# Kernel optimization log

Hardware: AMD Instinct MI355X
Metric: run time of the kernel (lower is better)

## Reference

```python
import jax, jax.numpy as jnp
import numpy as np

N_HEAD, D_MODEL, D_K, D_V = 16, 1024, 64, 64
B, S = 2, 2048
LN_EPS = 1e-5


def setup_inputs() -> dict:
    key = jax.random.key(0)
    ks = jax.random.split(key, 9)
    std_qk = np.sqrt(2.0 / (D_MODEL + D_K)).astype(np.float32)
    std_v = np.sqrt(2.0 / (D_MODEL + D_V)).astype(np.float32)
    return {
        "q": jax.random.normal(ks[0], (B, S, D_MODEL), jnp.float32),
        "k": jax.random.normal(ks[1], (B, S, D_MODEL), jnp.float32),
        "v": jax.random.normal(ks[2], (B, S, D_MODEL), jnp.float32),
        # nn.Linear weights stored as [out, in]; we apply x @ W.T
        "w_qs": jax.random.normal(ks[3], (N_HEAD * D_K, D_MODEL), jnp.float32) * std_qk,
        "w_ks": jax.random.normal(ks[4], (N_HEAD * D_K, D_MODEL), jnp.float32) * std_qk,
        "w_vs": jax.random.normal(ks[5], (N_HEAD * D_V, D_MODEL), jnp.float32) * std_v,
        "fc_w": jax.random.normal(ks[6], (D_MODEL, N_HEAD * D_V), jnp.float32) * np.sqrt(2.0 / (D_MODEL + N_HEAD * D_V)).astype(np.float32),
        "fc_b": jnp.zeros((D_MODEL,), jnp.float32),
        "ln_g": jnp.ones((D_MODEL,), jnp.float32),
        "ln_b": jnp.zeros((D_MODEL,), jnp.float32),
    }


def reference(q, k, v, w_qs, w_ks, w_vs, fc_w, fc_b, ln_g, ln_b):
    temperature = jnp.asarray(np.power(D_K, 0.5), q.dtype)
    residual = q
    # projections -> [b, s, h, d]
    qh = (q @ w_qs.T).reshape(B, S, N_HEAD, D_K)
    kh = (k @ w_ks.T).reshape(B, S, N_HEAD, D_K)
    vh = (v @ w_vs.T).reshape(B, S, N_HEAD, D_V)
    # scaled dot-product attention (dropout = identity in eval)
    attn = jnp.einsum('bqhd,bkhd->bhqk', qh, kh) / temperature
    attn = jax.nn.softmax(attn, axis=-1)  # (log_softmax in source is unused)
    out = jnp.einsum('bhqk,bkhd->bqhd', attn, vh).reshape(B, S, N_HEAD * D_V)
    out = out @ fc_w.T + fc_b
    # layer norm over last dim
    x = out + residual
    mu = jnp.mean(x, axis=-1, keepdims=True)
    var = jnp.var(x, axis=-1, keepdims=True)
    return (x - mu) * jax.lax.rsqrt(var + LN_EPS) * ln_g + ln_b
```

## Files before the change

### kernel.cpp

```cpp
#include <hip/hip_runtime.h>
#include <hip/hip_bf16.h>

typedef _Float16 f16x8 __attribute__((ext_vector_type(8)));
typedef _Float16 f16x4 __attribute__((ext_vector_type(4)));
typedef _Float16 f16x2 __attribute__((ext_vector_type(2)));
typedef float f32x4 __attribute__((ext_vector_type(4)));
typedef float f32x16 __attribute__((ext_vector_type(16)));
typedef unsigned u32x4v __attribute__((ext_vector_type(4)));
typedef int i32x2 __attribute__((ext_vector_type(2)));

#define DEVI __device__ __forceinline__

constexpr int S_LEN = 2048;
constexpr int DM    = 1024;
constexpr int NH    = 16;
constexpr int DHD   = 64;
constexpr int MTOT  = 2 * S_LEN;

DEVI f32x4 mfma16(f16x8 a, f16x8 b, f32x4 c) {
    return __builtin_amdgcn_mfma_f32_16x16x32_f16(a, b, c, 0, 0, 0);
}
DEVI f32x16 mfma32(f16x8 a, f16x8 b, f32x16 c) {
    return __builtin_amdgcn_mfma_f32_32x32x16_f16(a, b, c, 0, 0, 0);
}

DEVI f16x2 cvt_pk(float a, float b) {
    return __builtin_bit_cast(f16x2, __builtin_amdgcn_cvt_pkrtz(a, b));
}

DEVI float fexp2(float x) {
#if __has_builtin(__builtin_amdgcn_exp2f)
    return __builtin_amdgcn_exp2f(x);
#else
    return exp2f(x);
#endif
}

DEVI void pl32swap(unsigned &a, unsigned &b) {
#if __has_builtin(__builtin_amdgcn_permlane32_swap)
    i32x2 r = __builtin_bit_cast(i32x2,
        __builtin_amdgcn_permlane32_swap((int)a, (int)b, false, false));
    a = (unsigned)r[0]; b = (unsigned)r[1];
#else
    int idx = (((int)(threadIdx.x & 63)) ^ 32) << 2;
    unsigned ra = (unsigned)__builtin_amdgcn_ds_bpermute(idx, (int)a);
    unsigned rb = (unsigned)__builtin_amdgcn_ds_bpermute(idx, (int)b);
    bool hi = (threadIdx.x & 32) != 0;
    unsigned na = hi ? rb : a;
    unsigned nb = hi ? b  : ra;
    a = na; b = nb;
#endif
}

DEVI void gload_lds16(const _Float16* g, _Float16* l) {
    __builtin_amdgcn_global_load_lds(
        (const __attribute__((address_space(1))) void*)g,
        (__attribute__((address_space(3))) void*)l, 16, 0, 0);
}

__global__ void k_conv(const float* __restrict__ s0, const float* __restrict__ s1,
                       const float* __restrict__ s2, const float* __restrict__ s3,
                       const float* __restrict__ s4, const float* __restrict__ s5,
                       const float* __restrict__ s6,
                       _Float16* __restrict__ d0, _Float16* __restrict__ d1,
                       _Float16* __restrict__ d2, _Float16* __restrict__ d3,
                       _Float16* __restrict__ d4, _Float16* __restrict__ d5,
                       _Float16* __restrict__ d6)
{
    const int QN4 = (MTOT * DM) / 4;
    const int WN4 = (DM * DM) / 4;
    const int TOT = 3 * QN4 + 4 * WN4;
    int stride = gridDim.x * blockDim.x;
    for (int i = blockIdx.x * blockDim.x + threadIdx.x; i < TOT; i += stride) {
        const float* s; _Float16* d; int off;
        if (i < 3 * QN4) {
            int t = i / QN4; off = i - t * QN4;
            s = t == 0 ? s0 : (t == 1 ? s1 : s2);
            d = t == 0 ? d0 : (t == 1 ? d1 : d2);
        } else {
            int j = i - 3 * QN4;
            int t = j / WN4; off = j - t * WN4;
            s = t == 0 ? s3 : (t == 1 ? s4 : (t == 2 ? s5 : s6));
            d = t == 0 ? d3 : (t == 1 ? d4 : (t == 2 ? d5 : d6));
        }
        float4 v = reinterpret_cast<const float4*>(s)[off];
        f16x4 o;
        o[0] = (_Float16)v.x; o[1] = (_Float16)v.y;
        o[2] = (_Float16)v.z; o[3] = (_Float16)v.w;
        *reinterpret_cast<f16x4*>(d + (size_t)off * 4) = o;
    }
}

DEVI void gemm_main(const _Float16* __restrict__ A, const _Float16* __restrict__ Bw,
                    int kLen, int ld, int m0, int n0, f32x4 (&acc)[4][4])
{
    __shared__ __align__(16) _Float16 As[128 * 64];
    __shared__ __align__(16) _Float16 Bs[128 * 64];

    const int tid = threadIdx.x;
    const int lane = tid & 63;
    const int w = tid >> 6;
    const int wm = w >> 1, wn = w & 1;
    const int lrow = lane & 15, lg = lane >> 4;
    const int srow = w * 8 + (lane >> 3);
    const int scol = ((lane & 7) ^ (srow & 7)) * 8;

#pragma unroll
    for (int i = 0; i < 4; i++)
#pragma unroll
        for (int j = 0; j < 4; j++) acc[i][j] = f32x4{0.f, 0.f, 0.f, 0.f};

    const _Float16* gA = A  + (size_t)(m0 + srow) * ld + scol;
    const _Float16* gB = Bw + (size_t)(n0 + srow) * ld + scol;

#pragma unroll
    for (int q = 0; q < 4; q++) {
        gload_lds16(gA + (size_t)q * 32 * ld, &As[(w * 8 + q * 32) * 64]);
        gload_lds16(gB + (size_t)q * 32 * ld, &Bs[(w * 8 + q * 32) * 64]);
    }

    const int kTiles = kLen >> 6;
    for (int kt = 0; kt < kTiles; ++kt) {
        __syncthreads();
#pragma unroll
        for (int kk = 0; kk < 2; kk++) {
            f16x8 af[4], bfm[4];
#pragma unroll
            for (int i = 0; i < 4; i++) {
                int row = wm * 64 + i * 16 + lrow;
                int slot = (kk * 4 + lg) ^ (row & 7);
                af[i] = *reinterpret_cast<const f16x8*>(As + row * 64 + slot * 8);
            }
#pragma unroll
            for (int j = 0; j < 4; j++) {
                int row = wn * 64 + j * 16 + lrow;
                int slot = (kk * 4 + lg) ^ (row & 7);
                bfm[j] = *reinterpret_cast<const f16x8*>(Bs + row * 64 + slot * 8);
            }
#pragma unroll
            for (int i = 0; i < 4; i++)
#pragma unroll
                for (int j = 0; j < 4; j++)
                    acc[i][j] = mfma16(af[i], bfm[j], acc[i][j]);
        }
        if (kt + 1 < kTiles) {
            asm volatile("s_waitcnt lgkmcnt(0)" ::: "memory");
            __builtin_amdgcn_s_barrier();
            const int ko = (kt + 1) * 64;
#pragma unroll
            for (int q = 0; q < 4; q++) {
                gload_lds16(gA + ko + (size_t)q * 32 * ld, &As[(w * 8 + q * 32) * 64]);
                gload_lds16(gB + ko + (size_t)q * 32 * ld, &Bs[(w * 8 + q * 32) * 64]);
            }
        }
    }
}

__global__ __launch_bounds__(256, 4)
void k_proj(const _Float16* __restrict__ qb, const _Float16* __restrict__ kb,
            const _Float16* __restrict__ vb,
            const _Float16* __restrict__ wq, const _Float16* __restrict__ wk,
            const _Float16* __restrict__ wv,
            _Float16* __restrict__ Qh, _Float16* __restrict__ Ks, _Float16* __restrict__ Vs)
{
    const int z = blockIdx.z;
    const _Float16* A = z == 0 ? qb : (z == 1 ? kb : vb);
    const _Float16* B = z == 0 ? wq : (z == 1 ? wk : wv);
    const int m0 = blockIdx.x * 128, n0 = blockIdx.y * 128;
    f32x4 acc[4][4];
    gemm_main(A, B, DM, DM, m0, n0, acc);

    const int lane = threadIdx.x & 63, w = threadIdx.x >> 6;
    const int wm = w >> 1, wn = w & 1;
    const int lrow = lane & 15, lg = lane >> 4;

    if (z == 0) {
        const float scale = 0.18033688011112042f;
#pragma unroll
        for (int i = 0; i < 4; i++)
#pragma unroll
            for (int j = 0; j < 4; j++) {
                int n = n0 + wn * 64 + j * 16 + lrow;
                int h = n >> 6, d = n & 63;
#pragma unroll
                for (int r = 0; r < 4; r++) {
                    int m = m0 + wm * 64 + i * 16 + lg * 4 + r;
                    int b = m >> 11, s = m & (S_LEN - 1);
                    size_t idx = ((size_t)(b * NH + h) * S_LEN + s) * DHD + d;
                    Qh[idx] = (_Float16)(acc[i][j][r] * scale);
                }
            }
    } else if (z == 1) {
#pragma unroll
        for (int i = 0; i < 4; i++)
#pragma unroll
            for (int j = 0; j < 4; j++) {
                int n = n0 + wn * 64 + j * 16 + lrow;
                int h = n >> 6, d = n & 63;
#pragma unroll
                for (int r = 0; r < 4; r++) {
                    int m = m0 + wm * 64 + i * 16 + lg * 4 + r;
                    int b = m >> 11, s = m & (S_LEN - 1);
                    size_t idx = (size_t)(b * NH + h) * 131072
                               + (size_t)(s >> 6) * 4096
                               + (d >> 3) * 512 + (s & 63) * 8 + (d & 7);
                    Ks[idx] = (_Float16)acc[i][j][r];
                }
            }
    } else {
#pragma unroll
        for (int i = 0; i < 4; i++) {
            int m = m0 + wm * 64 + i * 16 + lg * 4;
            int b = m >> 11, s = m & (S_LEN - 1);
#pragma unroll
            for (int j = 0; j < 4; j++) {
                int n = n0 + wn * 64 + j * 16 + lrow;
                int h = n >> 6, d = n & 63;
                size_t idx = (size_t)(b * NH + h) * 131072
                           + (size_t)(s >> 6) * 4096
                           + ((s >> 3) & 7) * 512 + d * 8 + (s & 7);
                f16x4 pk;
#pragma unroll
                for (int r = 0; r < 4; r++) pk[r] = (_Float16)acc[i][j][r];
                *reinterpret_cast<f16x4*>(Vs + idx) = pk;
            }
        }
    }
}

__global__ __launch_bounds__(256, 2)
void k_attn(const _Float16* __restrict__ Q, const _Float16* __restrict__ Ks,
            const _Float16* __restrict__ Vs, _Float16* __restrict__ Ob)
{
    __shared__ __align__(16) _Float16 Kl[2][4096];
    __shared__ __align__(16) _Float16 Vl[2][4096];

    const int tid  = threadIdx.x;
    const int lane = tid & 63, w = tid >> 6;
    const int l31  = lane & 31, hh = lane >> 5;

    const int raw  = blockIdx.x;
    const int swz  = (raw & 7) * 64 + (raw >> 3);
    const int bh   = swz >> 4;
    const int qblk = swz & 15;
    const int q0   = qblk * 128 + w * 32;

    const _Float16* Qb = Q  + (size_t)bh * S_LEN * DHD;
    const _Float16* gK = Ks + (size_t)bh * 131072 + w * 1024 + lane * 8;
    const _Float16* gV = Vs + (size_t)bh * 131072 + w * 1024 + lane * 8;

    f16x8 qf[4];
#pragma unroll
    for (int step = 0; step < 4; step++)
        qf[step] = *reinterpret_cast<const f16x8*>(
            Qb + (size_t)(q0 + l31) * DHD + step * 16 + hh * 8);

    f32x16 oacc[2], lacc, cinit;
#pragma unroll
    for (int i = 0; i < 16; i++) {
        oacc[0][i] = 0.f; oacc[1][i] = 0.f; lacc[i] = 0.f; cinit[i] = -7.f;
    }
    f16x8 vones;
#pragma unroll
    for (int i = 0; i < 8; i++) vones[i] = (_Float16)1.0f;

#pragma unroll
    for (int i = 0; i < 2; i++) {
        gload_lds16(gK + i * 512, &Kl[0][w * 1024 + i * 512]);
        gload_lds16(gV + i * 512, &Vl[0][w * 1024 + i * 512]);
    }

    for (int t = 0; t < 32; ++t) {
        const int cur = t & 1;
        asm volatile("s_waitcnt vmcnt(0) lgkmcnt(0)" ::: "memory");
        __builtin_amdgcn_s_barrier();
        if (t + 1 < 32) {
#pragma unroll
            for (int i = 0; i < 2; i++) {
                gload_lds16(gK + (t + 1) * 4096 + i * 512, &Kl[cur ^ 1][w * 1024 + i * 512]);
                gload_lds16(gV + (t + 1) * 4096 + i * 512, &Vl[cur ^ 1][w * 1024 + i * 512]);
            }
        }
        const _Float16* Kc = Kl[cur];
        const _Float16* Vc = Vl[cur];

        f32x16 sc0 = cinit, sc1 = cinit;
        __builtin_amdgcn_s_setprio(1);
#pragma unroll
        for (int step = 0; step < 4; step++) {
            const int sl = step * 2 + hh;
            f16x8 ka = *reinterpret_cast<const f16x8*>(Kc + sl * 512 + l31 * 8);
            f16x8 kb = *reinterpret_cast<const f16x8*>(Kc + sl * 512 + 256 + l31 * 8);
            sc0 = mfma32(ka, qf[step], sc0);
            sc1 = mfma32(kb, qf[step], sc1);
        }
        __builtin_amdgcn_s_setprio(0);

#pragma unroll
        for (int kb2 = 0; kb2 < 2; kb2++) {
            const f32x16 sc = kb2 ? sc1 : sc0;
            float e[16];
#pragma unroll
            for (int r = 0; r < 16; r++) e[r] = fexp2(sc[r]);
            unsigned Wa[4], Wb[4];
#pragma unroll
            for (int g = 0; g < 4; g++) {
                Wa[g] = __builtin_bit_cast(unsigned, cvt_pk(e[4 * g],     e[4 * g + 1]));
                Wb[g] = __builtin_bit_cast(unsigned, cvt_pk(e[4 * g + 2], e[4 * g + 3]));
            }
            pl32swap(Wa[0], Wa[1]); pl32swap(Wb[0], Wb[1]);
            pl32swap(Wa[2], Wa[3]); pl32swap(Wb[2], Wb[3]);
#pragma unroll
            for (int win = 0; win < 2; win++) {
                u32x4v fw = {Wa[2 * win], Wb[2 * win], Wa[2 * win + 1], Wb[2 * win + 1]};
                f16x8 pa = __builtin_bit_cast(f16x8, fw);
                const int slotb = kb2 * 4 + win * 2 + hh;
                __builtin_amdgcn_s_setprio(1);
#pragma unroll
                for (int dblk = 0; dblk < 2; dblk++) {
                    f16x8 vf = *reinterpret_cast<const f16x8*>(
                        Vc + slotb * 512 + dblk * 256 + l31 * 8);
                    oacc[dblk] = mfma32(pa, vf, oacc[dblk]);
                }
                lacc = mfma32(pa, vones, lacc);
                __builtin_amdgcn_s_setprio(0);
            }
        }
    }

    const int b = bh >> 4, h = bh & 15;
#pragma unroll
    for (int r = 0; r < 16; r++) {
        const float iq = 1.0f / lacc[r];
        const int qrow = q0 + (r & 3) + 8 * (r >> 2) + 4 * hh;
        const size_t m = (size_t)(b * S_LEN + qrow) * DM + h * 64;
        Ob[m + l31]      = (_Float16)(oacc[0][r] * iq);
        Ob[m + 32 + l31] = (_Float16)(oacc[1][r] * iq);
    }
}

__global__ __launch_bounds__(256, 4)
void k_fc(const _Float16* __restrict__ Ob, const _Float16* __restrict__ Wfc,
          const float* __restrict__ bias,
          _Float16* __restrict__ fcoA, _Float16* __restrict__ fcoB)
{
    const int z = blockIdx.z;
    const int m0 = blockIdx.x * 128, n0 = blockIdx.y * 128;
    f32x4 acc[4][4];
    gemm_main(Ob + z * 512, Wfc + z * 512, 512, DM, m0, n0, acc);

    _Float16* out = z == 0 ? fcoA : fcoB;
    const int lane = threadIdx.x & 63, w = threadIdx.x >> 6;
    const int wm = w >> 1, wn = w & 1;
    const int lrow = lane & 15, lg = lane >> 4;
#pragma unroll
    for (int j = 0; j < 4; j++) {
        int n = n0 + wn * 64 + j * 16 + lrow;
        float bv = (z == 0) ? bias[n] : 0.f;
#pragma unroll
        for (int i = 0; i < 4; i++)
#pragma unroll
            for (int r = 0; r < 4; r++) {
                int m = m0 + wm * 64 + i * 16 + lg * 4 + r;
                out[(size_t)m * DM + n] = (_Float16)(acc[i][j][r] + bv);
            }
    }
}

__global__ void k_ln(const _Float16* __restrict__ fa, const _Float16* __restrict__ fb,
                     const float* __restrict__ res,
                     const float* __restrict__ g, const float* __restrict__ be,
                     float* __restrict__ out)
{
    int row = blockIdx.x * 4 + (threadIdx.x >> 6);
    int lane = threadIdx.x & 63;
    const f16x4* ar = reinterpret_cast<const f16x4*>(fa + (size_t)row * DM);
    const f16x4* br2 = reinterpret_cast<const f16x4*>(fb + (size_t)row * DM);
    const float4* rr = reinterpret_cast<const float4*>(res + (size_t)row * DM);
    float4 v[4];
    float sum = 0.f, sq = 0.f;
#pragma unroll
    for (int t = 0; t < 4; t++) {
        f16x4 a = ar[lane + 64 * t];
        f16x4 bq = br2[lane + 64 * t];
        float4 b = rr[lane + 64 * t];
        float4 c = make_float4((float)a[0] + (float)bq[0] + b.x,
                               (float)a[1] + (float)bq[1] + b.y,
                               (float)a[2] + (float)bq[2] + b.z,
                               (float)a[3] + (float)bq[3] + b.w);
        v[t] = c;
        sum += c.x + c.y + c.z + c.w;
        sq  += c.x * c.x + c.y * c.y + c.z * c.z + c.w * c.w;
    }
#pragma unroll
    for (int o = 1; o < 64; o <<= 1) { sum += __shfl_xor(sum, o); sq += __shfl_xor(sq, o); }
    float mu = sum * (1.f / DM);
    float rstd = rsqrtf(fmaxf(sq * (1.f / DM) - mu * mu, 0.f) + 1e-5f);
    float4* orow = reinterpret_cast<float4*>(out + (size_t)row * DM);
    const float4* gr = reinterpret_cast<const float4*>(g);
    const float4* brr = reinterpret_cast<const float4*>(be);
#pragma unroll
    for (int t = 0; t < 4; t++) {
        float4 gg = gr[lane + 64 * t], bb = brr[lane + 64 * t];
        float4 c = v[t];
        orow[lane + 64 * t] = make_float4((c.x - mu) * rstd * gg.x + bb.x,
                                          (c.y - mu) * rstd * gg.y + bb.y,
                                          (c.z - mu) * rstd * gg.z + bb.z,
                                          (c.w - mu) * rstd * gg.w + bb.w);
    }
}

extern "C" void kernel_launch(void* const* d_in, const int* in_sizes, int n_in,
                              void* d_out, int out_size, void* d_ws, size_t ws_size,
                              hipStream_t stream)
{
    const float* q    = (const float*)d_in[0];
    const float* k    = (const float*)d_in[1];
    const float* v    = (const float*)d_in[2];
    const float* w_qs = (const float*)d_in[3];
    const float* w_ks = (const float*)d_in[4];
    const float* w_vs = (const float*)d_in[5];
    const float* fc_w = (const float*)d_in[6];
    const float* fc_b = (const float*)d_in[7];
    const float* ln_g = (const float*)d_in[8];
    const float* ln_b = (const float*)d_in[9];
    float* out = (float*)d_out;

    if (ws_size < (size_t)67108864) return;

    _Float16* ws  = (_Float16*)d_ws;
    _Float16* qbf = ws;
    _Float16* kbf = qbf + 4194304;
    _Float16* vbf = kbf + 4194304;
    _Float16* wq  = vbf + 4194304;
    _Float16* wk  = wq + 1048576;
    _Float16* wv  = wk + 1048576;
    _Float16* wfc = wv + 1048576;
    _Float16* Qh  = wfc + 1048576;
    _Float16* Ks  = Qh + 4194304;
    _Float16* Vs  = Ks + 4194304;
    _Float16* Ob  = Vs + 4194304;
    _Float16* fcoA = qbf;
    _Float16* fcoB = kbf;

    k_conv<<<2048, 256, 0, stream>>>(q, k, v, w_qs, w_ks, w_vs, fc_w,
                                     qbf, kbf, vbf, wq, wk, wv, wfc);
    k_proj<<<dim3(32, 8, 3), 256, 0, stream>>>(qbf, kbf, vbf, wq, wk, wv, Qh, Ks, Vs);
    k_attn<<<512, 256, 0, stream>>>(Qh, Ks, Vs, Ob);
    k_fc<<<dim3(32, 8, 2), 256, 0, stream>>>(Ob, wfc, fc_b, fcoA, fcoB);
    k_ln<<<1024, 256, 0, stream>>>(fcoA, fcoB, q, ln_g, ln_b, out);
}
```

Baseline: 125.2 us.

## Split attention over two key halves and combine partial sums in a new kernel

The attention kernel now splits the key/value sequence in two along a second grid dimension, doubling the block count, and raises the occupancy hint to four blocks per CU. Each half writes an unnormalized fp16 output plus its row sums, and a new combine kernel adds the halves and divides by the total sum. This works without rescaling because softmax uses a fixed shift (-7) rather than a running max. The aim is more parallelism and occupancy; the cost is an extra launch, extra global traffic for the partial outputs, and some fp16 precision loss on the unnormalized partials.

```diff
diff --git a/kernel.cpp b/kernel.cpp
--- a/kernel.cpp
+++ b/kernel.cpp
@@ -228,9 +228,11 @@
     }
 }
 
-__global__ __launch_bounds__(256, 2)
+__global__ __launch_bounds__(256, 4)
 void k_attn(const _Float16* __restrict__ Q, const _Float16* __restrict__ Ks,
-            const _Float16* __restrict__ Vs, _Float16* __restrict__ Ob)
+            const _Float16* __restrict__ Vs,
+            _Float16* __restrict__ O0u, _Float16* __restrict__ O1u,
+            float* __restrict__ ls)
 {
     __shared__ __align__(16) _Float16 Kl[2][4096];
     __shared__ __align__(16) _Float16 Vl[2][4096];
@@ -238,6 +240,7 @@
     const int tid  = threadIdx.x;
     const int lane = tid & 63, w = tid >> 6;
     const int l31  = lane & 31, hh = lane >> 5;
+    const int z    = blockIdx.y;
 
     const int raw  = blockIdx.x;
     const int swz  = (raw & 7) * 64 + (raw >> 3);
@@ -245,9 +248,9 @@
     const int qblk = swz & 15;
     const int q0   = qblk * 128 + w * 32;
 
-    const _Float16* Qb = Q  + (size_t)bh * S_LEN * DHD;
-    const _Float16* gK = Ks + (size_t)bh * 131072 + w * 1024 + lane * 8;
-    const _Float16* gV = Vs + (size_t)bh * 131072 + w * 1024 + lane * 8;
+    const _Float16* Qb = Q + (size_t)bh * S_LEN * DHD;
+    const _Float16* gK = Ks + (size_t)bh * 131072 + (size_t)z * 65536 + w * 1024 + lane * 8;
+    const _Float16* gV = Vs + (size_t)bh * 131072 + (size_t)z * 65536 + w * 1024 + lane * 8;
 
     f16x8 qf[4];
 #pragma unroll
@@ -270,11 +273,11 @@
         gload_lds16(gV + i * 512, &Vl[0][w * 1024 + i * 512]);
     }
 
-    for (int t = 0; t < 32; ++t) {
+    for (int t = 0; t < 16; ++t) {
         const int cur = t & 1;
         asm volatile("s_waitcnt vmcnt(0) lgkmcnt(0)" ::: "memory");
         __builtin_amdgcn_s_barrier();
-        if (t + 1 < 32) {
+        if (t + 1 < 16) {
 #pragma unroll
             for (int i = 0; i < 2; i++) {
                 gload_lds16(gK + (t + 1) * 4096 + i * 512, &Kl[cur ^ 1][w * 1024 + i * 512]);
@@ -328,15 +331,39 @@
         }
     }
 
+    _Float16* Op = z ? O1u : O0u;
     const int b = bh >> 4, h = bh & 15;
 #pragma unroll
     for (int r = 0; r < 16; r++) {
-        const float iq = 1.0f / lacc[r];
         const int qrow = q0 + (r & 3) + 8 * (r >> 2) + 4 * hh;
         const size_t m = (size_t)(b * S_LEN + qrow) * DM + h * 64;
-        Ob[m + l31]      = (_Float16)(oacc[0][r] * iq);
-        Ob[m + 32 + l31] = (_Float16)(oacc[1][r] * iq);
-    }
+        Op[m + l31]      = (_Float16)oacc[0][r];
+        Op[m + 32 + l31] = (_Float16)oacc[1][r];
+    }
+    if (l31 == 0) {
+        float* lp = ls + (size_t)z * 65536 + (size_t)bh * S_LEN;
+#pragma unroll
+        for (int r = 0; r < 16; r++)
+            lp[q0 + (r & 3) + 8 * (r >> 2) + 4 * hh] = lacc[r];
+    }
+}
+
+__global__ void k_comb(const _Float16* __restrict__ O0u, _Float16* __restrict__ O1u,
+                       const float* __restrict__ ls)
+{
+    const int row  = blockIdx.x * 2 + (threadIdx.x >> 7);
+    const int col8 = (threadIdx.x & 127) * 8;
+    const int b = row >> 11, q = row & (S_LEN - 1);
+    const int h = col8 >> 6;
+    const size_t lidx = (size_t)(b * NH + h) * S_LEN + q;
+    const float inv = 1.0f / (ls[lidx] + ls[65536 + lidx]);
+    const size_t o = (size_t)row * DM + col8;
+    f16x8 a = *reinterpret_cast<const f16x8*>(O0u + o);
+    f16x8 c = *reinterpret_cast<const f16x8*>(O1u + o);
+    f16x8 r;
+#pragma unroll
+    for (int i = 0; i < 8; i++) r[i] = (_Float16)(((float)a[i] + (float)c[i]) * inv);
+    *reinterpret_cast<f16x8*>(O1u + o) = r;
 }
 
 __global__ __launch_bounds__(256, 4)
@@ -442,11 +469,15 @@
     _Float16* Ob  = Vs + 4194304;
     _Float16* fcoA = qbf;
     _Float16* fcoB = kbf;
+    _Float16* O0u  = vbf;
+    _Float16* O1u  = Ob;
+    float*    lsum = (float*)wq;
 
     k_conv<<<2048, 256, 0, stream>>>(q, k, v, w_qs, w_ks, w_vs, fc_w,
                                      qbf, kbf, vbf, wq, wk, wv, wfc);
     k_proj<<<dim3(32, 8, 3), 256, 0, stream>>>(qbf, kbf, vbf, wq, wk, wv, Qh, Ks, Vs);
-    k_attn<<<512, 256, 0, stream>>>(Qh, Ks, Vs, Ob);
+    k_attn<<<dim3(512, 2), 256, 0, stream>>>(Qh, Ks, Vs, O0u, O1u, lsum);
+    k_comb<<<2048, 256, 0, stream>>>(O0u, O1u, lsum);
     k_fc<<<dim3(32, 8, 2), 256, 0, stream>>>(Ob, wfc, fc_b, fcoA, fcoB);
     k_ln<<<1024, 256, 0, stream>>>(fcoA, fcoB, q, ln_g, ln_b, out);
 }
```

New measurement: 129.0 us (median of 2 runs). 3.0% more time.
